# Optimization experiments

Hardware: AMD Instinct MI355X
Metric: run time of the kernel (lower is better)

Reference implementation:

```python
import jax, jax.numpy as jnp
import numpy as np
from jax import lax

B, T, V, P, L = 16, 1024, 4096, 100, 128
BLANK = 0
TEMPERATURE = 1.0


def setup_inputs() -> dict:
    key = jax.random.key(0)
    k1, k2, k3, k4, k5 = jax.random.split(key, 5)
    emissions = jax.random.normal(k1, (B, T, V), dtype=jnp.float32)
    emissions_lengths = jax.random.randint(k2, (B,), T // 2, T + 1).astype(jnp.int32)
    labels = jax.random.randint(k3, (B, L), 1, V).astype(jnp.int32)  # non-blank tokens
    labels_length = jax.random.randint(k4, (B,), L // 2, L + 1).astype(jnp.int32)
    paths = jax.random.randint(k5, (B, P, T), 0, V).astype(jnp.int32)  # sampled lattice paths
    return {"emissions": emissions, "emissions_lengths": emissions_lengths,
            "labels": labels, "labels_length": labels_length, "paths": paths}


def _edit_distance(paths, valid, labels, labels_length):
    """Levenshtein distance between each CTC-collapsed path and its reference.
    paths/valid: (B,P,T) int/bool; labels: (B,L); returns (B,P) int32."""
    refs = labels[:, None, :]                       # (B,1,L)
    js = jnp.arange(L + 1, dtype=jnp.int32)
    D0 = jnp.broadcast_to(js, (B, P, L + 1))        # D[j]=j: j insertions

    def step(D, inp):
        c, v = inp                                  # c: (B,P) token, v: (B,P) valid flag
        sub = (refs != c[..., None]).astype(jnp.int32)          # (B,P,L)
        cand_rest = jnp.minimum(D[..., 1:] + 1, D[..., :-1] + sub)
        cand = jnp.concatenate([D[..., :1] + 1, cand_rest], axis=-1)  # (B,P,L+1)
        # insertion closure: new[j] = min_{k<=j} cand[k] + (j-k), via prefix-min trick
        run = lax.associative_scan(jnp.minimum, cand - js, axis=-1)
        new = run + js
        return jnp.where(v[..., None], new, D), None

    toks = jnp.moveaxis(paths, 2, 0)                # (T,B,P)
    vals = jnp.moveaxis(valid, 2, 0)                # (T,B,P)
    D, _ = lax.scan(step, D0, (toks, vals))
    idx = jnp.broadcast_to(labels_length[:, None, None].astype(jnp.int32), (B, P, 1))
    return jnp.take_along_axis(D, idx, axis=-1)[..., 0]  # (B,P)


def reference(emissions, emissions_lengths, labels, labels_length, paths):
    logp = jax.nn.log_softmax(emissions, axis=-1)                   # (B,T,V)
    frame_mask = jnp.arange(T) < emissions_lengths[:, None]          # (B,T)
    # path total log-prob: gather logp at each path token per frame
    idx = jnp.swapaxes(paths, 1, 2)                                  # (B,T,P)
    g = jnp.take_along_axis(logp, idx, axis=2)                       # (B,T,P)
    scores = jnp.sum(g * frame_mask[:, :, None], axis=1)             # (B,P)
    posterior = jax.nn.softmax(scores / TEMPERATURE, axis=1)         # per-utterance path posterior
    # CTC collapse: drop blanks and consecutive repeats
    prev = jnp.concatenate([jnp.full((B, P, 1), -1, paths.dtype), paths[..., :-1]], axis=-1)
    valid = (paths != BLANK) & (paths != prev) & frame_mask[:, None, :]
    wers = _edit_distance(paths, valid, labels, labels_length).astype(logp.dtype)  # (B,P)
    # MWER (eq. 2): expected edit distance under path posterior, reduction='sum'
    return jnp.sum(posterior * wers)
```

## Files before the change

kernel.cpp:

```cpp
#include <hip/hip_runtime.h>
#include <stdint.h>

#define B 16
#define T 1024
#define V 4096
#define P 100
#define L 128

__global__ __launch_bounds__(256) void scores4_kernel(
    const float* __restrict__ emissions,
    const int* __restrict__ emissions_lengths,
    const int* __restrict__ paths,
    float* __restrict__ scores_part)
{
    int gid = blockIdx.x * blockDim.x + threadIdx.x;
    int wave = gid >> 6;
    int lane = threadIdx.x & 63;
    if (wave >= B * P * 4) return;
    int w  = wave & 3;
    int bp = wave >> 2;
    int b  = bp / P;
    int len = emissions_lengths[b];
    const int4* path4 = (const int4*)(paths + (size_t)bp * T);
    int4 tk = path4[w * 64 + lane];
    int tbase = 4 * (w * 64 + lane);
    const float* em = emissions + (size_t)b * T * V;

    float acc = 0.f;
    if (tbase + 0 < len) acc += em[(size_t)(tbase + 0) * V + tk.x];
    if (tbase + 1 < len) acc += em[(size_t)(tbase + 1) * V + tk.y];
    if (tbase + 2 < len) acc += em[(size_t)(tbase + 2) * V + tk.z];
    if (tbase + 3 < len) acc += em[(size_t)(tbase + 3) * V + tk.w];

    #pragma unroll
    for (int off = 32; off; off >>= 1) acc += __shfl_down(acc, off, 64);
    if (lane == 0) scores_part[bp * 4 + w] = acc;
}

__global__ __launch_bounds__(256) void wer_kernel(
    const int* __restrict__ emissions_lengths,
    const int* __restrict__ labels,
    const int* __restrict__ labels_length,
    const int* __restrict__ paths,
    float* __restrict__ wers)
{
    __shared__ unsigned short toks[4][1024];
    int gid = blockIdx.x * blockDim.x + threadIdx.x;
    int wave = gid >> 6;
    int lane = threadIdx.x & 63;
    int slot = (threadIdx.x >> 6) & 3;
    if (wave >= B * P) return;
    int b = wave / P;
    int len = emissions_lengths[b];
    int ll  = labels_length[b];
    const int* path = paths + (size_t)wave * T;

    int prev_last = -1;
    int base = 0;
    for (int t0 = 0; t0 < len; t0 += 64) {
        int c = path[t0 + lane];
        int cp = __shfl_up(c, 1, 64);
        if (lane == 0) cp = prev_last;
        bool valid = (c != 0) && (c != cp) && (t0 + lane < len);
        unsigned long long mask = __ballot(valid);
        int pos = base + __popcll(mask & ((1ull << lane) - 1ull));
        if (valid) toks[slot][pos] = (unsigned short)c;
        base += __popcll(mask);
        prev_last = __shfl(c, 63, 64);
    }
    int S = base;

    int j1 = 2 * lane + 1;
    int j2 = 2 * lane + 2;
    int r1 = labels[b * L + 2 * lane];
    int r2 = labels[b * L + 2 * lane + 1];

    int A1 = j1, B1 = j1;
    int A2 = j2, B2 = j2;
    int tok1 = 0, tok2 = 0;
    int tnext = toks[slot][(1 - 2 * lane - 2) & 1023];
    int dmax = S + ll;

    for (int d = 1; d <= dmax; d++) {
        int packed = (A2 << 16) | B2;
        int up = __shfl_up(packed, 1, 64);
        int upA, upB;
        if (lane == 0) { upA = d - 1; upB = d - 2; }
        else { upA = ((unsigned)up) >> 16; upB = up & 0xffff; }

        tok2 = tok1;
        tok1 = tnext;
        tnext = toks[slot][(d + 1 - 2 * lane - 2) & 1023];

        int t1 = d - j1;
        int n1 = min(min(A1, upA) + 1, upB + (tok1 != r1));
        if (t1 <= 0) n1 = j1;
        else if (t1 > S) n1 = A1;

        int t2 = d - j2;
        int n2 = min(min(A2, A1) + 1, B1 + (tok2 != r2));
        if (t2 <= 0) n2 = j2;
        else if (t2 > S) n2 = A2;

        B1 = A1; A1 = n1;
        B2 = A2; A2 = n2;
    }

    int va = __shfl(A1, (ll - 1) >> 1, 64);
    int vb = __shfl(A2, (ll - 2) >> 1, 64);
    int res = (ll & 1) ? va : vb;
    if (lane == 0) wers[wave] = (float)res;
}

__global__ __launch_bounds__(1024) void reduce_kernel(
    const float* __restrict__ scores_part,
    const float* __restrict__ wers,
    float* __restrict__ out)
{
    __shared__ float contrib[B];
    int lane = threadIdx.x & 63;
    int b = threadIdx.x >> 6;

    int p1 = b * P + lane;
    float s1 = scores_part[p1 * 4 + 0] + scores_part[p1 * 4 + 1]
             + scores_part[p1 * 4 + 2] + scores_part[p1 * 4 + 3];
    float w1 = wers[p1];
    bool has2 = lane < (P - 64);
    int p2 = b * P + 64 + (has2 ? lane : 0);
    float s2 = has2 ? (scores_part[p2 * 4 + 0] + scores_part[p2 * 4 + 1]
                     + scores_part[p2 * 4 + 2] + scores_part[p2 * 4 + 3])
                    : -3.4e38f;
    float w2 = has2 ? wers[p2] : 0.f;

    float m = fmaxf(s1, s2);
    #pragma unroll
    for (int off = 32; off; off >>= 1) m = fmaxf(m, __shfl_xor(m, off, 64));
    float e1 = expf(s1 - m);
    float e2 = has2 ? expf(s2 - m) : 0.f;
    float num = e1 * w1 + e2 * w2;
    float den = e1 + e2;
    #pragma unroll
    for (int off = 32; off; off >>= 1) {
        num += __shfl_xor(num, off, 64);
        den += __shfl_xor(den, off, 64);
    }
    if (lane == 0) contrib[b] = num / den;
    __syncthreads();
    if (threadIdx.x == 0) {
        float s = 0.f;
        #pragma unroll
        for (int i = 0; i < B; i++) s += contrib[i];
        out[0] = s;
    }
}

extern "C" void kernel_launch(void* const* d_in, const int* in_sizes, int n_in,
                              void* d_out, int out_size, void* d_ws, size_t ws_size,
                              hipStream_t stream) {
    const float* emissions          = (const float*)d_in[0];
    const int*   emissions_lengths  = (const int*)d_in[1];
    const int*   labels             = (const int*)d_in[2];
    const int*   labels_length      = (const int*)d_in[3];
    const int*   paths              = (const int*)d_in[4];
    float* out = (float*)d_out;

    float* scores_part = (float*)d_ws;
    float* wers        = scores_part + B * P * 4;

    scores4_kernel<<<(B * P * 4 * 64) / 256, 256, 0, stream>>>(
        emissions, emissions_lengths, paths, scores_part);
    wer_kernel<<<(B * P * 64) / 256, 256, 0, stream>>>(
        emissions_lengths, labels, labels_length, paths, wers);
    reduce_kernel<<<1, 1024, 0, stream>>>(scores_part, wers, out);
}
```

Baseline: 491.1 us.

## Process two paths per wave in edit-distance DP with unrolled DPP steps

The wavefront edit-distance kernel now has each wave handle two paths, interleaving their anti-diagonal recurrences so the two independent dependency chains can hide each other's latency. The diagonal loop is unrolled by four with token prefetch from LDS, the cross-lane shift uses a DPP row-shift instead of shfl, and the boundary branches are replaced by a max with a clamp expression plus capture of the final diagonal value. Path compaction loads all 16 chunks up front. The scores kernel's block-to-(b,p) mapping is also permuted across XCDs. This halves the wave count, which lowers occupancy, and the loop runs to the larger of the two paths' lengths.

```diff
diff --git a/kernel.cpp b/kernel.cpp
--- a/kernel.cpp
+++ b/kernel.cpp
@@ -13,12 +13,9 @@
     const int* __restrict__ paths,
     float* __restrict__ scores_part)
 {
-    int gid = blockIdx.x * blockDim.x + threadIdx.x;
-    int wave = gid >> 6;
+    int bp = 200 * (blockIdx.x & 7) + (blockIdx.x >> 3);
+    int w  = threadIdx.x >> 6;
     int lane = threadIdx.x & 63;
-    if (wave >= B * P * 4) return;
-    int w  = wave & 3;
-    int bp = wave >> 2;
     int b  = bp / P;
     int len = emissions_lengths[b];
     const int4* path4 = (const int4*)(paths + (size_t)bp * T);
@@ -36,6 +33,21 @@
     for (int off = 32; off; off >>= 1) acc += __shfl_down(acc, off, 64);
     if (lane == 0) scores_part[bp * 4 + w] = acc;
 }
+
+#define STEP(S, d, newtok) do {                                              \
+    int packed = (A2##S << 16) | B2##S;                                      \
+    int up = __builtin_amdgcn_update_dpp(0, packed, 0x138, 0xF, 0xF, true);  \
+    int upA = lane ? (int)(((unsigned)up) >> 16) : ((d) - 1);                \
+    int upB = lane ? (up & 0xffff)               : ((d) - 2);                \
+    tok2##S = tok1##S; tok1##S = (newtok);                                   \
+    int n1 = min(min(A1##S, upA) + 1, upB + (tok1##S != r1));                \
+    n1 = max(n1, cj1 - (d));                                                 \
+    int n2 = min(min(A2##S, A1##S) + 1, B1##S + (tok2##S != r2));            \
+    n2 = max(n2, cj2 - (d));                                                 \
+    B1##S = A1##S; A1##S = n1; B2##S = A2##S; A2##S = n2;                    \
+} while (0)
+
+#define CAP(S, d) do { if ((d) == dmax##S) { rA1##S = A1##S; rA2##S = A2##S; } } while (0)
 
 __global__ __launch_bounds__(256) void wer_kernel(
     const int* __restrict__ emissions_lengths,
@@ -44,72 +56,89 @@
     const int* __restrict__ paths,
     float* __restrict__ wers)
 {
-    __shared__ unsigned short toks[4][1024];
-    int gid = blockIdx.x * blockDim.x + threadIdx.x;
-    int wave = gid >> 6;
+    __shared__ unsigned short toks[8][1024];
+    int wid  = blockIdx.x * 4 + (threadIdx.x >> 6);
     int lane = threadIdx.x & 63;
-    int slot = (threadIdx.x >> 6) & 3;
-    if (wave >= B * P) return;
-    int b = wave / P;
+    int b = wid / (P / 2);
+    int q = wid % (P / 2);
     int len = emissions_lengths[b];
     int ll  = labels_length[b];
-    const int* path = paths + (size_t)wave * T;
-
-    int prev_last = -1;
-    int base = 0;
-    for (int t0 = 0; t0 < len; t0 += 64) {
-        int c = path[t0 + lane];
-        int cp = __shfl_up(c, 1, 64);
-        if (lane == 0) cp = prev_last;
-        bool valid = (c != 0) && (c != cp) && (t0 + lane < len);
-        unsigned long long mask = __ballot(valid);
-        int pos = base + __popcll(mask & ((1ull << lane) - 1ull));
-        if (valid) toks[slot][pos] = (unsigned short)c;
-        base += __popcll(mask);
-        prev_last = __shfl(c, 63, 64);
-    }
-    int S = base;
+    const int* pathA = paths + (size_t)(b * P + 2 * q) * T;
+    const int* pathB = pathA + T;
+    unsigned short* tkA = toks[(threadIdx.x >> 6) * 2 + 0];
+    unsigned short* tkB = toks[(threadIdx.x >> 6) * 2 + 1];
+    unsigned long long lt = (1ull << lane) - 1ull;
+
+    auto compact = [&](const int* __restrict__ path,
+                       unsigned short* __restrict__ dst) -> int {
+        int c[16];
+        #pragma unroll
+        for (int k = 0; k < 16; k++) c[k] = path[k * 64 + lane];
+        int prev_last = -1, base = 0;
+        #pragma unroll
+        for (int k = 0; k < 16; k++) {
+            int cc = c[k];
+            int cp = __builtin_amdgcn_update_dpp(0, cc, 0x138, 0xF, 0xF, true);
+            if (lane == 0) cp = prev_last;
+            bool valid = (cc != 0) && (cc != cp) && (k * 64 + lane < len);
+            unsigned long long mask = __ballot(valid);
+            int pos = base + __popcll(mask & lt);
+            if (valid) dst[pos] = (unsigned short)cc;
+            base += __popcll(mask);
+            prev_last = __builtin_amdgcn_readlane(cc, 63);
+        }
+        return base;
+    };
+    int Sa = compact(pathA, tkA);
+    int Sb = compact(pathB, tkB);
 
     int j1 = 2 * lane + 1;
     int j2 = 2 * lane + 2;
     int r1 = labels[b * L + 2 * lane];
     int r2 = labels[b * L + 2 * lane + 1];
-
-    int A1 = j1, B1 = j1;
-    int A2 = j2, B2 = j2;
-    int tok1 = 0, tok2 = 0;
-    int tnext = toks[slot][(1 - 2 * lane - 2) & 1023];
-    int dmax = S + ll;
-
-    for (int d = 1; d <= dmax; d++) {
-        int packed = (A2 << 16) | B2;
-        int up = __shfl_up(packed, 1, 64);
-        int upA, upB;
-        if (lane == 0) { upA = d - 1; upB = d - 2; }
-        else { upA = ((unsigned)up) >> 16; upB = up & 0xffff; }
-
-        tok2 = tok1;
-        tok1 = tnext;
-        tnext = toks[slot][(d + 1 - 2 * lane - 2) & 1023];
-
-        int t1 = d - j1;
-        int n1 = min(min(A1, upA) + 1, upB + (tok1 != r1));
-        if (t1 <= 0) n1 = j1;
-        else if (t1 > S) n1 = A1;
-
-        int t2 = d - j2;
-        int n2 = min(min(A2, A1) + 1, B1 + (tok2 != r2));
-        if (t2 <= 0) n2 = j2;
-        else if (t2 > S) n2 = A2;
-
-        B1 = A1; A1 = n1;
-        B2 = A2; A2 = n2;
-    }
-
-    int va = __shfl(A1, (ll - 1) >> 1, 64);
-    int vb = __shfl(A2, (ll - 2) >> 1, 64);
-    int res = (ll & 1) ? va : vb;
-    if (lane == 0) wers[wave] = (float)res;
+    int cj1 = 2 * j1;
+    int cj2 = 2 * j2;
+    int tb = -2 * lane - 2;
+
+    int A1a = j1, B1a = j1, A2a = j2, B2a = j2, tok1a = 0, tok2a = 0;
+    int A1b = j1, B1b = j1, A2b = j2, B2b = j2, tok1b = 0, tok2b = 0;
+    int rA1a = j1, rA2a = j2, rA1b = j1, rA2b = j2;
+    int dmaxa = Sa + ll;
+    int dmaxb = Sb + ll;
+    int dmax = max(dmaxa, dmaxb);
+
+    int ca0 = tkA[(1 + tb) & 1023], ca1 = tkA[(2 + tb) & 1023];
+    int ca2 = tkA[(3 + tb) & 1023], ca3 = tkA[(4 + tb) & 1023];
+    int cb0 = tkB[(1 + tb) & 1023], cb1 = tkB[(2 + tb) & 1023];
+    int cb2 = tkB[(3 + tb) & 1023], cb3 = tkB[(4 + tb) & 1023];
+
+    for (int d = 1; d <= dmax; d += 4) {
+        int pa0 = tkA[(d + 4 + tb) & 1023];
+        int pa1 = tkA[(d + 5 + tb) & 1023];
+        int pa2 = tkA[(d + 6 + tb) & 1023];
+        int pa3 = tkA[(d + 7 + tb) & 1023];
+        int pb0 = tkB[(d + 4 + tb) & 1023];
+        int pb1 = tkB[(d + 5 + tb) & 1023];
+        int pb2 = tkB[(d + 6 + tb) & 1023];
+        int pb3 = tkB[(d + 7 + tb) & 1023];
+        STEP(a, d + 0, ca0); STEP(b, d + 0, cb0); CAP(a, d + 0); CAP(b, d + 0);
+        STEP(a, d + 1, ca1); STEP(b, d + 1, cb1); CAP(a, d + 1); CAP(b, d + 1);
+        STEP(a, d + 2, ca2); STEP(b, d + 2, cb2); CAP(a, d + 2); CAP(b, d + 2);
+        STEP(a, d + 3, ca3); STEP(b, d + 3, cb3); CAP(a, d + 3); CAP(b, d + 3);
+        ca0 = pa0; ca1 = pa1; ca2 = pa2; ca3 = pa3;
+        cb0 = pb0; cb1 = pb1; cb2 = pb2; cb3 = pb3;
+    }
+
+    int vaa = __shfl(rA1a, (ll - 1) >> 1, 64);
+    int vba = __shfl(rA2a, (ll - 2) >> 1, 64);
+    int resa = (ll & 1) ? vaa : vba;
+    int vab = __shfl(rA1b, (ll - 1) >> 1, 64);
+    int vbb = __shfl(rA2b, (ll - 2) >> 1, 64);
+    int resb = (ll & 1) ? vab : vbb;
+    if (lane == 0) {
+        wers[b * P + 2 * q + 0] = (float)resa;
+        wers[b * P + 2 * q + 1] = (float)resb;
+    }
 }
 
 __global__ __launch_bounds__(1024) void reduce_kernel(
@@ -169,7 +198,7 @@
 
     scores4_kernel<<<(B * P * 4 * 64) / 256, 256, 0, stream>>>(
         emissions, emissions_lengths, paths, scores_part);
-    wer_kernel<<<(B * P * 64) / 256, 256, 0, stream>>>(
+    wer_kernel<<<(B * P / 2 * 64) / 256, 256, 0, stream>>>(
         emissions_lengths, labels, labels_length, paths, wers);
     reduce_kernel<<<1, 1024, 0, stream>>>(scores_part, wers, out);
 }
```

New measurement: 453.1 us. -7.8%, faster.
